# Optimization experiments

Measured on AMD Instinct MI355X. Metric: run time of the kernel, lower is better.

The kernel has to match this reference:

```python
import jax, jax.numpy as jnp
import numpy as np


def _block_interconnect(x, c):
    # x: [B, L_in]; c: [n_blocks, block_in, block_out]
    n_blocks, block_in, block_out = c.shape
    conn = jax.nn.softmax(c, axis=1)  # softmax over block inputs
    xr = x.reshape(-1, n_blocks, block_in)
    out = jnp.einsum('bnm,nmo->bno', xr, conn)
    return out.reshape(x.shape[0], n_blocks * block_out)


def _gate16(x, w):
    # x: [B, 2*G] -> pairs (A, B); w: [16, G]
    Bsz = x.shape[0]
    G = w.shape[1]
    xp = x.reshape(Bsz, G, 2)
    A = xp[:, :, 0]
    Bv = xp[:, :, 1]
    AB = A * Bv
    S = A + Bv - AB  # OR
    zeros = jnp.zeros_like(A)
    ones = jnp.ones_like(A)
    gates = jnp.stack([
        zeros, AB, A - AB, A, Bv - AB, Bv, S - AB, S,
        1.0 - S, 1.0 - (S - AB), 1.0 - Bv, 1.0 - (Bv - AB),
        1.0 - A, 1.0 - (A - AB), 1.0 - AB, ones,
    ], axis=0)  # [16, B, G]
    ws = jax.nn.softmax(w, axis=0)  # [16, G]
    return jnp.einsum('kbg,kg->bg', gates, ws)  # [B, G]


def setup_inputs() -> dict:
    key = jax.random.key(0)
    ks = jax.random.split(key, 7)
    B = 16384
    return {
        'x': jax.random.uniform(ks[0], (B, 256), dtype=jnp.float32),
        'c0': jax.random.normal(ks[1], (8, 32, 325), dtype=jnp.float32),
        'w0': jax.random.normal(ks[2], (16, 1300), dtype=jnp.float32),
        'c1': jax.random.normal(ks[3], (50, 26, 52), dtype=jnp.float32),
        'w1': jax.random.normal(ks[4], (16, 1300), dtype=jnp.float32),
        'c2': jax.random.normal(ks[5], (50, 26, 52), dtype=jnp.float32),
        'w2': jax.random.normal(ks[6], (16, 1300), dtype=jnp.float32),
    }


def reference(x, c0, w0, c1, w1, c2, w2):
    NUM_CATEGORIES = 10
    h = _block_interconnect(x, c0)   # [B, 2600]
    h = _gate16(h, w0)               # [B, 1300]
    h = _block_interconnect(h, c1)   # [B, 2600]
    h = _gate16(h, w1)               # [B, 1300]
    h = _block_interconnect(h, c2)   # [B, 2600]
    h = _gate16(h, w2)               # [B, 1300]
    logits = h.reshape(h.shape[0], NUM_CATEGORIES, -1).sum(axis=-1)  # [B, 10]
    return jax.nn.softmax(logits, axis=-1)
```

## Files before the change

kernel.cpp:

```cpp
#include <hip/hip_runtime.h>
#include <cstdint>

#define NT 768
#define NWAVE 12

static constexpr int W0T_OFF = 0;
static constexpr int W1T_OFF = 83200;
static constexpr int W2T_OFF = 150800;
static constexpr int CF_OFF  = 218400;
static constexpr int LG_OFF  = 234000;

__global__ void precompute_kernel(const float* __restrict__ c0,
                                  const float* __restrict__ w0,
                                  const float* __restrict__ c1,
                                  const float* __restrict__ w1,
                                  const float* __restrict__ c2,
                                  const float* __restrict__ w2,
                                  float* __restrict__ ws) {
  int id = blockIdx.x * blockDim.x + threadIdx.x;
  if (id < 2600) {
    int n = id / 325, o = id - n * 325;
    const float* src = c0 + n * (32 * 325) + o;
    float v[32]; float mx = -3.4e38f;
#pragma unroll
    for (int m = 0; m < 32; ++m) { v[m] = src[m * 325]; mx = fmaxf(mx, v[m]); }
    float ssum = 0.f;
#pragma unroll
    for (int m = 0; m < 32; ++m) { v[m] = __expf(v[m] - mx); ssum += v[m]; }
    float inv = 1.f / ssum;
    float* dst = ws + W0T_OFF + (n * 325 + o) * 32;
#pragma unroll
    for (int m = 0; m < 32; ++m) dst[m] = v[m] * inv;
    return;
  }
  id -= 2600;
  if (id < 5200) {
    const float* src0 = (id < 2600) ? c1 : c2;
    float* dst0 = ws + ((id < 2600) ? W1T_OFF : W2T_OFF);
    int col = (id < 2600) ? id : id - 2600;
    int k = col / 52, o = col - k * 52;
    const float* src = src0 + k * (26 * 52) + o;
    float v[26]; float mx = -3.4e38f;
#pragma unroll
    for (int m = 0; m < 26; ++m) { v[m] = src[m * 52]; mx = fmaxf(mx, v[m]); }
    float ssum = 0.f;
#pragma unroll
    for (int m = 0; m < 26; ++m) { v[m] = __expf(v[m] - mx); ssum += v[m]; }
    float inv = 1.f / ssum;
    float* dst = dst0 + (k * 52 + o) * 26;
#pragma unroll
    for (int m = 0; m < 26; ++m) dst[m] = v[m] * inv;
    return;
  }
  id -= 5200;
  if (id < 3900) {
    int layer = id / 1300, g = id - layer * 1300;
    const float* w = (layer == 0) ? w0 : ((layer == 1) ? w1 : w2);
    float v[16]; float mx = -3.4e38f;
#pragma unroll
    for (int k = 0; k < 16; ++k) { v[k] = w[k * 1300 + g]; mx = fmaxf(mx, v[k]); }
    float ssum = 0.f;
#pragma unroll
    for (int k = 0; k < 16; ++k) { v[k] = __expf(v[k] - mx); ssum += v[k]; }
    float inv = 1.f / ssum;
#pragma unroll
    for (int k = 0; k < 16; ++k) v[k] *= inv;
    float alpha = v[8] + v[9] + v[10] + v[11] + v[12] + v[13] + v[14] + v[15];
    float beta  = v[2] + v[3] + v[6] + v[7] - v[8] - v[9] - v[12] - v[13];
    float gamma = v[4] + v[5] + v[6] + v[7] - v[8] - v[9] - v[10] - v[11];
    float delta = v[1] - v[2] - v[4] - 2.f * v[6] - v[7] + v[8] + 2.f * v[9]
                + v[11] + v[13] - v[14];
    reinterpret_cast<float4*>(ws + CF_OFF)[id] =
        make_float4(alpha, beta, gamma, delta);
  }
}

__device__ __forceinline__ float gate4(float4 cv, float a0, float a1) {
  return fmaf(cv.w, a0 * a1, fmaf(cv.z, a1, fmaf(cv.y, a0, cv.x)));
}

static constexpr int XB_FLOATS = 64 * 257;
static constexpr int LG_FLOATS = 64 * 5;

__global__ __launch_bounds__(NT, 6) void chain_kernel(
    const float* __restrict__ x, const float* __restrict__ ws,
    float* __restrict__ lgout, int B) {
  extern __shared__ float smem[];
  float* xb  = smem;
  float* lgb = smem + XB_FLOATS;
  const int tid = threadIdx.x;
  const int sblk = blockIdx.x >> 1;
  const int half = blockIdx.x & 1;
  const int s0 = sblk * 64;

  {
    const float4* x4 = reinterpret_cast<const float4*>(x);
    for (int idx = tid; idx < 64 * 64; idx += NT) {
      int r = idx >> 6, c4 = idx & 63;
      float4 v = make_float4(0.f, 0.f, 0.f, 0.f);
      if (s0 + r < B) v = x4[(size_t)(s0 + r) * 64 + c4];
      float* d = &xb[r * 257 + c4 * 4];
      d[0] = v.x; d[1] = v.y; d[2] = v.z; d[3] = v.w;
    }
    for (int i = tid; i < LG_FLOATS; i += NT) lgb[i] = 0.f;
  }
  __syncthreads();

  const int lane = tid & 63;
  const int wv = __builtin_amdgcn_readfirstlane(tid >> 6);
  const float* w0T = ws + W0T_OFF;
  const float* w1T = ws + W1T_OFF;
  const float* w2T = ws + W2T_OFF;
  const float4* cf = reinterpret_cast<const float4*>(ws + CF_OFF);
  const float* xrow = xb + lane * 257;

  const int cnt = (wv == 0) ? 3 : 2;
  const int cst = 25 * half + ((wv == 0) ? 0 : (1 + 2 * wv));

  for (int ci = 0; ci < cnt; ++ci) {
    const int K = cst + ci;
    const int cs = 52 * K;
    const int nlo = cs / 325;
    const int nhi = (cs + 51) / 325;
    const int split = (nhi > nlo) ? (325 * nhi - cs) : 52;
    const int t1 = split >> 1;
    const int odd = split & 1;
    const float4* cfK = cf + 26 * K;

    float h[26];
    float inp[32];
#pragma unroll
    for (int j = 0; j < 32; ++j) inp[j] = xrow[nlo * 32 + j];

#pragma unroll
    for (int P = 0; P < 26; ++P) {
      if (P < t1) {
        const float* wp = w0T + (size_t)(nlo * 325 + (cs - 325 * nlo) + 2 * P) * 32;
        float a0 = 0.f, a1 = 0.f;
#pragma unroll
        for (int j = 0; j < 32; ++j) {
          a0 = fmaf(inp[j], wp[j], a0);
          a1 = fmaf(inp[j], wp[32 + j], a1);
        }
        h[P] = gate4(cfK[P], a0, a1);
      }
    }
    if (nhi > nlo) {
      float a0s = 0.f, a1s = 0.f, gs = 0.f;
      if (odd) {
        const float* wp = w0T + (size_t)(nlo * 325 + (cs - 325 * nlo) + 2 * t1) * 32;
#pragma unroll
        for (int j = 0; j < 32; ++j) a0s = fmaf(inp[j], wp[j], a0s);
      }
#pragma unroll
      for (int j = 0; j < 32; ++j) inp[j] = xrow[nhi * 32 + j];
      if (odd) {
        const float* wq = w0T + (size_t)(nhi * 325) * 32;
#pragma unroll
        for (int j = 0; j < 32; ++j) a1s = fmaf(inp[j], wq[j], a1s);
        gs = gate4(cf[26 * K + t1], a0s, a1s);
      }
#pragma unroll
      for (int P = 0; P < 26; ++P) {
        if (P >= t1 + odd) {
          const float* wp = w0T + (size_t)(nhi * 325 + (cs - 325 * nhi) + 2 * P) * 32;
          float a0 = 0.f, a1 = 0.f;
#pragma unroll
          for (int j = 0; j < 32; ++j) {
            a0 = fmaf(inp[j], wp[j], a0);
            a1 = fmaf(inp[j], wp[32 + j], a1);
          }
          h[P] = gate4(cfK[P], a0, a1);
        }
      }
      if (odd) {
#pragma unroll
        for (int P = 0; P < 26; ++P)
          if (P == t1) h[P] = gs;
      }
    }

    float h2[26];
    {
      const float* wb = w1T + (size_t)K * (52 * 26);
      const float4* cf1 = cf + 1300 + 26 * K;
#pragma unroll
      for (int q = 0; q < 26; ++q) {
        const float* wp = wb + q * 52;
        float a0 = 0.f, a1 = 0.f;
#pragma unroll
        for (int j = 0; j < 26; ++j) {
          a0 = fmaf(h[j], wp[j], a0);
          a1 = fmaf(h[j], wp[26 + j], a1);
        }
        h2[q] = gate4(cf1[q], a0, a1);
      }
    }

    float psum = 0.f;
    {
      const float* wb = w2T + (size_t)K * (52 * 26);
      const float4* cf2 = cf + 2600 + 26 * K;
#pragma unroll 1
      for (int q = 0; q < 26; ++q) {
        const float* wp = wb + q * 52;
        float a0 = 0.f, a1 = 0.f;
#pragma unroll
        for (int j = 0; j < 26; ++j) {
          a0 = fmaf(h2[j], wp[j], a0);
          a1 = fmaf(h2[j], wp[26 + j], a1);
        }
        float4 cv = cf2[q];
        psum += gate4(cv, a0, a1);
      }
    }
    atomicAdd(&lgb[lane * 5 + (K / 5 - 5 * half)], psum);
  }
  __syncthreads();

  for (int i = tid; i < LG_FLOATS; i += NT) {
    int s = i / 5, c = i - (i / 5) * 5;
    if (s0 + s < B) lgout[(size_t)(s0 + s) * 10 + 5 * half + c] = lgb[i];
  }
}

__global__ __launch_bounds__(256) void softmax_kernel(
    const float* __restrict__ lgin, float* __restrict__ out, int B) {
  int s = blockIdx.x * 256 + threadIdx.x;
  if (s >= B) return;
  float lg[10];
#pragma unroll
  for (int c = 0; c < 10; ++c) lg[c] = lgin[(size_t)s * 10 + c];
  float mx = lg[0];
#pragma unroll
  for (int c = 1; c < 10; ++c) mx = fmaxf(mx, lg[c]);
  float ssum = 0.f;
#pragma unroll
  for (int c = 0; c < 10; ++c) { lg[c] = __expf(lg[c] - mx); ssum += lg[c]; }
  float inv = 1.f / ssum;
  float* o = out + (size_t)s * 10;
#pragma unroll
  for (int c = 0; c < 10; ++c) o[c] = lg[c] * inv;
}

extern "C" void kernel_launch(void* const* d_in, const int* in_sizes, int n_in,
                              void* d_out, int out_size, void* d_ws, size_t ws_size,
                              hipStream_t stream) {
  const float* x  = (const float*)d_in[0];
  const float* c0 = (const float*)d_in[1];
  const float* w0 = (const float*)d_in[2];
  const float* c1 = (const float*)d_in[3];
  const float* w1 = (const float*)d_in[4];
  const float* c2 = (const float*)d_in[5];
  const float* w2 = (const float*)d_in[6];
  float* out = (float*)d_out;
  float* ws  = (float*)d_ws;
  const int B = in_sizes[0] / 256;

  precompute_kernel<<<46, 256, 0, stream>>>(c0, w0, c1, w1, c2, w2, ws);

  const size_t smem_bytes = (size_t)(XB_FLOATS + LG_FLOATS) * sizeof(float);
  hipFuncSetAttribute(reinterpret_cast<const void*>(chain_kernel),
                      hipFuncAttributeMaxDynamicSharedMemorySize, (int)smem_bytes);
  const int nblk = (B + 63) / 64;
  chain_kernel<<<nblk * 2, NT, smem_bytes, stream>>>(x, ws, ws + LG_OFF, B);
  softmax_kernel<<<(B + 255) / 256, 256, 0, stream>>>(ws + LG_OFF, out, B);
}
```

Baseline: 171.7 us.

## Split each sample tile across four smaller workgroups with reduced x staging

Each 64-sample tile is now split across four 512-thread workgroups instead of two 768-thread ones. Each workgroup owns 15 or 10 output chunks and stages only the input column blocks those chunks need into a narrower LDS buffer. The goal is to cut LDS footprint per workgroup, raise occupancy and spread work more evenly across waves. It also partially unrolls the last layer loop. In exchange, overlapping x column blocks are loaded redundantly across workgroups and the load is unbalanced (some waves handle 2 chunks, others 1).

Result: faster. 164.5 us (-4.2%).

```diff
diff --git a/kernel.cpp b/kernel.cpp
--- a/kernel.cpp
+++ b/kernel.cpp
@@ -1,8 +1,7 @@
 #include <hip/hip_runtime.h>
 #include <cstdint>
 
-#define NT 768
-#define NWAVE 12
+#define NT 512
 
 static constexpr int W0T_OFF = 0;
 static constexpr int W1T_OFF = 83200;
@@ -79,30 +78,41 @@
   return fmaf(cv.w, a0 * a1, fmaf(cv.z, a1, fmaf(cv.y, a0, cv.x)));
 }
 
-static constexpr int XB_FLOATS = 64 * 257;
-static constexpr int LG_FLOATS = 64 * 5;
-
-__global__ __launch_bounds__(NT, 6) void chain_kernel(
+static constexpr int XB_STRIDE = 98;
+static constexpr int XB_FLOATS = 64 * XB_STRIDE;
+static constexpr int LG_FLOATS = 64 * 3;
+
+__global__ __launch_bounds__(NT, 8) void chain_kernel(
     const float* __restrict__ x, const float* __restrict__ ws,
     float* __restrict__ lgout, int B) {
   extern __shared__ float smem[];
   float* xb  = smem;
   float* lgb = smem + XB_FLOATS;
   const int tid = threadIdx.x;
-  const int sblk = blockIdx.x >> 1;
-  const int half = blockIdx.x & 1;
-  const int s0 = sblk * 64;
+  const int bid = blockIdx.x;
+  const int tile = bid >> 2;
+  const int half = (bid >> 1) & 1;
+  const int sub = bid & 1;
+  const int s0 = tile * 64;
+
+  const int base = half * 25 + sub * 15;
+  const int cnt_wg = sub ? 10 : 15;
+  const int clsbase = half * 5 + sub * 3;
+  const int nlgc = sub ? 2 : 3;
+  const int bl0 = (52 * base) / 325;
+  const int nb = (52 * (base + cnt_wg) - 1) / 325 - bl0 + 1;
 
   {
     const float4* x4 = reinterpret_cast<const float4*>(x);
-    for (int idx = tid; idx < 64 * 64; idx += NT) {
-      int r = idx >> 6, c4 = idx & 63;
+    const int rowq = nb * 8;
+    for (int idx = tid; idx < 64 * rowq; idx += NT) {
+      int r = idx / rowq, c4 = idx - r * rowq;
       float4 v = make_float4(0.f, 0.f, 0.f, 0.f);
-      if (s0 + r < B) v = x4[(size_t)(s0 + r) * 64 + c4];
-      float* d = &xb[r * 257 + c4 * 4];
+      if (s0 + r < B) v = x4[(size_t)(s0 + r) * 64 + bl0 * 8 + c4];
+      float* d = &xb[r * XB_STRIDE + c4 * 4];
       d[0] = v.x; d[1] = v.y; d[2] = v.z; d[3] = v.w;
     }
-    for (int i = tid; i < LG_FLOATS; i += NT) lgb[i] = 0.f;
+    for (int i = tid; i < 64 * nlgc; i += NT) lgb[i] = 0.f;
   }
   __syncthreads();
 
@@ -112,13 +122,15 @@
   const float* w1T = ws + W1T_OFF;
   const float* w2T = ws + W2T_OFF;
   const float4* cf = reinterpret_cast<const float4*>(ws + CF_OFF);
-  const float* xrow = xb + lane * 257;
-
-  const int cnt = (wv == 0) ? 3 : 2;
-  const int cst = 25 * half + ((wv == 0) ? 0 : (1 + 2 * wv));
-
-  for (int ci = 0; ci < cnt; ++ci) {
-    const int K = cst + ci;
+  const float* xrow = xb + lane * XB_STRIDE;
+
+  int cw, start;
+  if (sub == 0) { cw = (wv < 7) ? 2 : 1; start = 2 * wv; }
+  else          { cw = (wv < 2) ? 2 : 1; start = (wv < 2) ? 2 * wv : 2 + wv; }
+
+#pragma unroll 1
+  for (int ci = 0; ci < cw; ++ci) {
+    const int K = base + start + ci;
     const int cs = 52 * K;
     const int nlo = cs / 325;
     const int nhi = (cs + 51) / 325;
@@ -130,7 +142,7 @@
     float h[26];
     float inp[32];
 #pragma unroll
-    for (int j = 0; j < 32; ++j) inp[j] = xrow[nlo * 32 + j];
+    for (int j = 0; j < 32; ++j) inp[j] = xrow[(nlo - bl0) * 32 + j];
 
 #pragma unroll
     for (int P = 0; P < 26; ++P) {
@@ -153,7 +165,7 @@
         for (int j = 0; j < 32; ++j) a0s = fmaf(inp[j], wp[j], a0s);
       }
 #pragma unroll
-      for (int j = 0; j < 32; ++j) inp[j] = xrow[nhi * 32 + j];
+      for (int j = 0; j < 32; ++j) inp[j] = xrow[(nhi - bl0) * 32 + j];
       if (odd) {
         const float* wq = w0T + (size_t)(nhi * 325) * 32;
 #pragma unroll
@@ -201,7 +213,7 @@
     {
       const float* wb = w2T + (size_t)K * (52 * 26);
       const float4* cf2 = cf + 2600 + 26 * K;
-#pragma unroll 1
+#pragma unroll 2
       for (int q = 0; q < 26; ++q) {
         const float* wp = wb + q * 52;
         float a0 = 0.f, a1 = 0.f;
@@ -210,17 +222,16 @@
           a0 = fmaf(h2[j], wp[j], a0);
           a1 = fmaf(h2[j], wp[26 + j], a1);
         }
-        float4 cv = cf2[q];
-        psum += gate4(cv, a0, a1);
-      }
-    }
-    atomicAdd(&lgb[lane * 5 + (K / 5 - 5 * half)], psum);
+        psum += gate4(cf2[q], a0, a1);
+      }
+    }
+    atomicAdd(&lgb[lane * nlgc + (K / 5 - clsbase)], psum);
   }
   __syncthreads();
 
-  for (int i = tid; i < LG_FLOATS; i += NT) {
-    int s = i / 5, c = i - (i / 5) * 5;
-    if (s0 + s < B) lgout[(size_t)(s0 + s) * 10 + 5 * half + c] = lgb[i];
+  for (int i = tid; i < 64 * nlgc; i += NT) {
+    int s = i / nlgc, c = i - (i / nlgc) * nlgc;
+    if (s0 + s < B) lgout[(size_t)(s0 + s) * 10 + clsbase + c] = lgb[i];
   }
 }
 
@@ -263,6 +274,6 @@
   hipFuncSetAttribute(reinterpret_cast<const void*>(chain_kernel),
                       hipFuncAttributeMaxDynamicSharedMemorySize, (int)smem_bytes);
   const int nblk = (B + 63) / 64;
-  chain_kernel<<<nblk * 2, NT, smem_bytes, stream>>>(x, ws, ws + LG_OFF, B);
+  chain_kernel<<<nblk * 4, NT, smem_bytes, stream>>>(x, ws, ws + LG_OFF, B);
   softmax_kernel<<<(B + 255) / 256, 256, 0, stream>>>(ws + LG_OFF, out, B);
 }
```
